# Kernel tuning notes

Measured on AMD Instinct MI355X. Metric: run time of the kernel, lower is better.

Reference implementation:

```python
import jax, jax.numpy as jnp
import numpy as np

N = 8388608  # batch size

def _xor(a, b):
    return a + b - 2.0 * a * b

def _or(a, b):
    return a + b - a * b

def setup_inputs() -> dict:
    key = jax.random.key(0)
    k1, k2 = jax.random.split(key)
    # binary 0/1 inputs as float32 (SNN spike values)
    A = jnp.round(jax.random.uniform(k1, (N, 8), dtype=jnp.float32))
    B = jnp.round(jax.random.uniform(k2, (N, 8), dtype=jnp.float32))
    Bin = jnp.zeros((N, 1), dtype=jnp.float32)
    return {"A": A, "B": B, "Bin": Bin}

def reference(A, B, Bin):
    """8-bit ripple-borrow subtractor A - B. Index 7 is the LSB.
    XOR(a,b)=a+b-2ab, AND=ab, OR=a+b-ab, NOT=1-a on 0/1 values."""
    borrow = Bin  # [N, 1]
    diffs = [None] * 8
    for i in range(7, -1, -1):  # LSB (7) -> MSB (0)
        a_i = A[..., i:i + 1]
        b_i = B[..., i:i + 1]
        diff = _xor(_xor(a_i, b_i), borrow)
        not_a = 1.0 - a_i
        borrow = _or(_or(not_a * b_i, not_a * borrow), b_i * borrow)
        diffs[i] = diff
    return jnp.concatenate(diffs, axis=-1), borrow
```

## Files before the change

kernel.cpp:

```cpp
#include <hip/hip_runtime.h>


typedef unsigned int u32;
typedef u32 u32x4 __attribute__((ext_vector_type(4)));
#define FONE 0x3F800000u

__global__ __launch_bounds__(256) void sub8_kernel(
    const u32x4* __restrict__ A4, const u32x4* __restrict__ B4,
    const u32* __restrict__ Bin, u32x4* __restrict__ D4,
    u32* __restrict__ Bout, int n2 )
{
    int t = blockIdx.x * blockDim.x + threadIdx.x;
    if (t >= n2) return;
    const bool odd = (t & 1) != 0;
    const int  r   = t >> 1;

    u32x4 a = A4[t];
    u32x4 b = B4[t];
    u32 binw = Bin[r];

    u32 av[4] = {a.x, a.y, a.z, a.w};
    u32 bv[4] = {b.x, b.y, b.z, b.w};
    u32 d0v[4], d1v[4];
    u32 bor0 = 0u, bor1 = FONE;
    #pragma unroll
    for (int j = 3; j >= 0; --j) {
        u32 na = av[j] ^ FONE;
        u32 x  = av[j] ^ bv[j];
        u32 g  = na & bv[j];
        u32 p  = na | bv[j];
        d0v[j] = x ^ bor0;
        d1v[j] = x ^ bor1;
        bor0 = g | (p & bor0);
        bor1 = g | (p & bor1);
    }

    u32 bout_low = binw ? bor1 : bor0;
    u32 xs = __shfl_xor(bout_low, 1);
    u32 myborrow = odd ? binw : xs;

    u32x4 d = myborrow ? (u32x4){d1v[0], d1v[1], d1v[2], d1v[3]}
                       : (u32x4){d0v[0], d0v[1], d0v[2], d0v[3]};
    D4[t] = d;

    if (!odd)
        Bout[r] = myborrow ? bor1 : bor0;
}

extern "C" void kernel_launch(void* const* d_in, const int* in_sizes, int n_in,
                              void* d_out, int out_size, void* d_ws, size_t ws_size,
                              hipStream_t stream) {
    const u32* A   = (const u32*)d_in[0];
    const u32* B   = (const u32*)d_in[1];
    const u32* Bin = (const u32*)d_in[2];
    int n  = in_sizes[0] / 8;
    int n2 = n * 2;

    u32* D    = (u32*)d_out;
    u32* Bout = D + (size_t)n * 8;

    const int block = 256;
    int grid = (n2 + block - 1) / block;

    sub8_kernel<<<grid, block, 0, stream>>>(
        (const u32x4*)A, (const u32x4*)B, Bin, (u32x4*)D, Bout, n2);
}
```

Before: 154.3 us.

## Process two full rows per thread instead of splitting rows across lane pairs

Each thread now handles two complete 8-bit rows with a plain serial ripple borrow. This removes the dual-borrow speculation and the cross-lane shuffle, and uses vector loads for the borrow-in and borrow-out words. The cost is that the 16-byte accesses within a wave become strided, which can hurt coalescing, and there are fewer threads in total. The bound check assumes an even row count.

```diff
diff --git a/kernel.cpp b/kernel.cpp
--- a/kernel.cpp
+++ b/kernel.cpp
@@ -3,48 +3,55 @@
 
 typedef unsigned int u32;
 typedef u32 u32x4 __attribute__((ext_vector_type(4)));
+typedef u32 u32x2 __attribute__((ext_vector_type(2)));
 #define FONE 0x3F800000u
+
+__device__ __forceinline__ void ripple8(const u32x4 hi, const u32x4 lo, 
+                                        const u32x4 bhi, const u32x4 blo,
+                                        u32 bin, u32x4& dhi, u32x4& dlo, u32& bout)
+{
+    u32 av[8] = {hi.x, hi.y, hi.z, hi.w, lo.x, lo.y, lo.z, lo.w};
+    u32 bv[8] = {bhi.x, bhi.y, bhi.z, bhi.w, blo.x, blo.y, blo.z, blo.w};
+    u32 dv[8];
+    u32 bor = bin;
+    #pragma unroll
+    for (int j = 7; j >= 0; --j) {
+        u32 x  = av[j] ^ bv[j];
+        u32 na = av[j] ^ FONE;
+        u32 g  = na & bv[j];
+        u32 p  = na | bv[j];
+        dv[j]  = x ^ bor;
+        bor    = g | (p & bor);
+    }
+    dhi = (u32x4){dv[0], dv[1], dv[2], dv[3]};
+    dlo = (u32x4){dv[4], dv[5], dv[6], dv[7]};
+    bout = bor;
+}
 
 __global__ __launch_bounds__(256) void sub8_kernel(
     const u32x4* __restrict__ A4, const u32x4* __restrict__ B4,
-    const u32* __restrict__ Bin, u32x4* __restrict__ D4,
-    u32* __restrict__ Bout, int n2 )
+    const u32x2* __restrict__ Bin2, u32x4* __restrict__ D4,
+    u32x2* __restrict__ Bout2, int nt )
 {
     int t = blockIdx.x * blockDim.x + threadIdx.x;
-    if (t >= n2) return;
-    const bool odd = (t & 1) != 0;
-    const int  r   = t >> 1;
+    if (t >= nt) return;
 
-    u32x4 a = A4[t];
-    u32x4 b = B4[t];
-    u32 binw = Bin[r];
+    u32x4 a0 = A4[4 * t],     a1 = A4[4 * t + 1];
+    u32x4 a2 = A4[4 * t + 2], a3 = A4[4 * t + 3];
+    u32x4 b0 = B4[4 * t],     b1 = B4[4 * t + 1];
+    u32x4 b2 = B4[4 * t + 2], b3 = B4[4 * t + 3];
+    u32x2 bin = Bin2[t];
 
-    u32 av[4] = {a.x, a.y, a.z, a.w};
-    u32 bv[4] = {b.x, b.y, b.z, b.w};
-    u32 d0v[4], d1v[4];
-    u32 bor0 = 0u, bor1 = FONE;
-    #pragma unroll
-    for (int j = 3; j >= 0; --j) {
-        u32 na = av[j] ^ FONE;
-        u32 x  = av[j] ^ bv[j];
-        u32 g  = na & bv[j];
-        u32 p  = na | bv[j];
-        d0v[j] = x ^ bor0;
-        d1v[j] = x ^ bor1;
-        bor0 = g | (p & bor0);
-        bor1 = g | (p & bor1);
-    }
+    u32x4 d0, d1, d2, d3;
+    u32 bo0, bo1;
+    ripple8(a0, a1, b0, b1, bin.x, d0, d1, bo0);
+    ripple8(a2, a3, b2, b3, bin.y, d2, d3, bo1);
 
-    u32 bout_low = binw ? bor1 : bor0;
-    u32 xs = __shfl_xor(bout_low, 1);
-    u32 myborrow = odd ? binw : xs;
-
-    u32x4 d = myborrow ? (u32x4){d1v[0], d1v[1], d1v[2], d1v[3]}
-                       : (u32x4){d0v[0], d0v[1], d0v[2], d0v[3]};
-    D4[t] = d;
-
-    if (!odd)
-        Bout[r] = myborrow ? bor1 : bor0;
+    D4[4 * t]     = d0;
+    D4[4 * t + 1] = d1;
+    D4[4 * t + 2] = d2;
+    D4[4 * t + 3] = d3;
+    Bout2[t] = (u32x2){bo0, bo1};
 }
 
 extern "C" void kernel_launch(void* const* d_in, const int* in_sizes, int n_in,
@@ -54,14 +61,15 @@
     const u32* B   = (const u32*)d_in[1];
     const u32* Bin = (const u32*)d_in[2];
     int n  = in_sizes[0] / 8;
-    int n2 = n * 2;
+    int nt = n / 2;
 
     u32* D    = (u32*)d_out;
     u32* Bout = D + (size_t)n * 8;
 
     const int block = 256;
-    int grid = (n2 + block - 1) / block;
+    int grid = (nt + block - 1) / block;
 
     sub8_kernel<<<grid, block, 0, stream>>>(
-        (const u32x4*)A, (const u32x4*)B, Bin, (u32x4*)D, Bout, n2);
+        (const u32x4*)A, (const u32x4*)B, (const u32x2*)Bin,
+        (u32x4*)D, (u32x2*)Bout, nt);
 }
```

Result: slower. 182.3 us (+18.1%).
